# Performance work log

Measured on AMD Instinct MI355X. Metric: run time of the kernel, lower is better.

Reference implementation:

```python
import jax, jax.numpy as jnp
import numpy as np

N_A, N_B = 50000, 20000   # authors, teams
E0, E1, E2 = 600000, 300000, 300000  # coauthor(A->A), writes(A->B), influences(B->A)
D = 128                   # in_feats = out_feats


def setup_inputs() -> dict:
    key = jax.random.key(0)
    ks = jax.random.split(key, 12)
    h_A = jax.random.normal(ks[0], (N_A, D), jnp.float32)
    h_B = jax.random.normal(ks[1], (N_B, D), jnp.float32)
    W0 = jax.random.normal(ks[2], (D, D), jnp.float32) * 0.05
    W1 = jax.random.normal(ks[3], (D, D), jnp.float32) * 0.05
    W2 = jax.random.normal(ks[4], (D, D), jnp.float32) * 0.05
    b0 = jnp.zeros((D,), jnp.float32)
    b1 = jnp.zeros((D,), jnp.float32)
    b2 = jnp.zeros((D,), jnp.float32)
    src0 = jax.random.randint(ks[5], (E0,), 0, N_A)
    dst0 = jax.random.randint(ks[6], (E0,), 0, N_A)
    src1 = jax.random.randint(ks[7], (E1,), 0, N_A)
    dst1 = jax.random.randint(ks[8], (E1,), 0, N_B)
    src2 = jax.random.randint(ks[9], (E2,), 0, N_B)
    dst2 = jax.random.randint(ks[10], (E2,), 0, N_A)
    return dict(h_A=h_A, h_B=h_B, W0=W0, b0=b0, W1=W1, b1=b1, W2=W2, b2=b2,
                src0=src0, dst0=dst0, src1=src1, dst1=dst1, src2=src2, dst2=dst2)


def _graph_conv(x_src, W, b, src, dst, n_dst):
    """DGL GraphConv, norm='both': out = D_dst^{-1/2} A D_src^{-1/2} (X W) + b."""
    n_src = x_src.shape[0]
    ones = jnp.ones(src.shape[0], x_src.dtype)
    deg_out = jnp.clip(jax.ops.segment_sum(ones, src, num_segments=n_src), 1.0)
    deg_in = jnp.clip(jax.ops.segment_sum(ones, dst, num_segments=n_dst), 1.0)
    m = (x_src @ W) * (deg_out ** -0.5)[:, None]          # [n_src, D]
    agg = jax.ops.segment_sum(m[src], dst, num_segments=n_dst)  # [n_dst, D]
    return agg * (deg_in ** -0.5)[:, None] + b


def reference(h_A, h_B, W0, b0, W1, b1, W2, b2, src0, dst0, src1, dst1, src2, dst2):
    # HeteroGraphConv(aggregate='sum'): sum per-relation GraphConv outputs per dst ntype.
    out_A = (_graph_conv(h_A, W0, b0, src0, dst0, N_A)
             + _graph_conv(h_B, W2, b2, src2, dst2, N_A))
    out_B = _graph_conv(h_A, W1, b1, src1, dst1, N_B)
    # every ntype present in h receives an output, so no passthrough branch fires
    return out_A, out_B
```

## Files before the change

kernel.cpp:

```cpp
#include <hip/hip_runtime.h>

#define NA 50000
#define NB 20000
#define NE0 600000
#define NE1 300000
#define NE2 300000
#define DD 128
#define SUB 32768
#define PER 18750


typedef short bf16x8 __attribute__((ext_vector_type(8)));
typedef float f32x4 __attribute__((ext_vector_type(4)));

__device__ __forceinline__ unsigned short f2bf(float f) {
    union { float f; unsigned int u; } v; v.f = f;
    unsigned int r = v.u + 0x7fffu + ((v.u >> 16) & 1u);
    return (unsigned short)(r >> 16);
}
__device__ __forceinline__ float lo2f(unsigned int u) {
    union { float f; unsigned int u; } v; v.u = u << 16;
    return v.f;
}
__device__ __forceinline__ float hi2f(unsigned int u) {
    union { float f; unsigned int u; } v; v.u = u & 0xffff0000u;
    return v.f;
}

__global__ __launch_bounds__(1024) void hist_kernel(
    const int* __restrict__ s0, const int* __restrict__ d0,
    const int* __restrict__ s1, const int* __restrict__ d1,
    const int* __restrict__ s2, const int* __restrict__ d2,
    unsigned int* __restrict__ Pd,
    unsigned char* __restrict__ rank0, unsigned char* __restrict__ rank1,
    unsigned char* __restrict__ rank2,
    const float* __restrict__ W0, const float* __restrict__ W1,
    const float* __restrict__ W2, unsigned short* __restrict__ Wt)
{
    __shared__ unsigned int h32[SUB / 2];
    const int cfg = blockIdx.z;
    if (cfg == 6) {
        int flat = blockIdx.y * 2 + blockIdx.x;
        if (flat >= 48) return;
        int i = flat * 1024 + threadIdx.x;
        int w = i >> 14, r = i & (DD * DD - 1);
        int c = r >> 7, k = r & (DD - 1);
        const float* W = (w == 0) ? W0 : ((w == 1) ? W1 : W2);
        Wt[i] = f2bf(W[k * DD + c]);
        return;
    }
    const int En[6] = {NE0, NE0, NE1, NE1, NE2, NE2};
    const int Kn[6] = {NA, NA, NA, NB, NB, NA};
    const int Gn[6] = {32, 32, 16, 16, 16, 16};
    const int Po[6] = {0, 1600000, 3200000, 4000000, 4320000, 4640000};
    int E = En[cfg], K = Kn[cfg], G = Gn[cfg];
    int sub = blockIdx.x, g = blockIdx.y;
    int nsub = (K + SUB - 1) / SUB;
    if (sub >= nsub || g >= G) return;
    const int* keys = cfg == 0 ? s0 : cfg == 1 ? d0 : cfg == 2 ? s1
                    : cfg == 3 ? d1 : cfg == 4 ? s2 : d2;
    unsigned char* rk = cfg == 1 ? rank0 : cfg == 3 ? rank1
                      : cfg == 5 ? rank2 : (unsigned char*)0;
    int lo = sub * SUB;
    int hi = min(K, lo + SUB);
    int cnt = hi - lo;
    for (int i = threadIdx.x; i < SUB / 2; i += 1024) h32[i] = 0;
    __syncthreads();
    int e1 = min(E, g * PER + PER);
    for (int e = g * PER + threadIdx.x; e < e1; e += 1024) {
        int k = keys[e];
        if (k >= lo && k < hi) {
            int kk = k - lo;
            unsigned sh = (kk & 1) << 4;
            unsigned old = atomicAdd(&h32[kk >> 1], 1u << sh);
            if (rk) rk[e] = (unsigned char)((old >> sh) & 0xffu);
        }
    }
    __syncthreads();
    unsigned int* outp = Pd + ((Po[cfg] + g * K + lo) >> 1);
    for (int i = threadIdx.x; i < cnt / 2; i += 1024) outp[i] = h32[i];
}

__global__ __launch_bounds__(256) void reduce2(
    const unsigned short* __restrict__ P16, int* __restrict__ ideg,
    float* __restrict__ rdeg, int* __restrict__ spart,
    unsigned char* __restrict__ cum8)
{
    __shared__ int lds[256];
    const int y = blockIdx.y;
    const int Ro[6] = {0, NA, 2 * NA, 3 * NA, 3 * NA + NB, 3 * NA + 2 * NB};
    const int Kr[6] = {NA, NA, NA, NB, NB, NA};
    const int Gr[6] = {32, 32, 16, 16, 16, 16};
    const int Po[6] = {0, 1600000, 3200000, 4000000, 4320000, 4640000};
    const int Co[6] = {0, 0, 0, 1600000, 0, 1920000};
    int K = Kr[y], G = Gr[y];
    int b = blockIdx.x, t = threadIdx.x;
    int nchunk = (K + 255) >> 8;
    if (b >= nchunk) return;
    int key = b * 256 + t;
    bool valid = key < K;
    bool din = (y == 1) || (y == 3) || (y == 5);
    const unsigned short* p = P16 + Po[y] + key;
    unsigned char* cb = cum8 + Co[y] + key;
    int run = 0;
    for (int g = 0; g < G; ++g) {
        if (din && valid) cb[g * K] = (unsigned char)run;
        run += valid ? p[g * K] : 0;
    }
    if (valid) {
        ideg[Ro[y] + key] = run;
        rdeg[Ro[y] + key] = rsqrtf(fmaxf((float)run, 1.f));
    }
    if (din) {
        int slot = (y - 1) >> 1;
        lds[t] = run; __syncthreads();
        for (int o = 128; o > 0; o >>= 1) {
            if (t < o) lds[t] += lds[t + o];
            __syncthreads();
        }
        if (t == 0) spart[slot * 256 + b] = lds[0];
    }
}

__global__ __launch_bounds__(256) void scan3(
    const int* __restrict__ ideg, const int* __restrict__ spart,
    int* __restrict__ rp)
{
    __shared__ int lds[256];
    const int y = blockIdx.y;
    const int off[3] = {NA, 3 * NA, 3 * NA + 2 * NB};
    const int nn[3]  = {NA, NB, NA};
    const int ro[3]  = {0, NA, NA + NB};
    int n = nn[y];
    int b = blockIdx.x, t = threadIdx.x;
    if (b * 1024 >= n) return;

    lds[t] = (t < 4 * b) ? spart[y * 256 + t] : 0;
    __syncthreads();
    for (int o = 128; o > 0; o >>= 1) {
        if (t < o) lds[t] += lds[t + o];
        __syncthreads();
    }
    int pv = lds[0];
    __syncthreads();

    const int* deg = ideg + off[y];
    int base = b * 1024 + t * 4;
    int v[4]; int tsum = 0;
    #pragma unroll
    for (int k = 0; k < 4; ++k) {
        v[k] = (base + k < n) ? deg[base + k] : 0;
        tsum += v[k];
    }
    lds[t] = tsum; __syncthreads();
    for (int o = 1; o < 256; o <<= 1) {
        int x = (t >= o) ? lds[t - o] : 0;
        __syncthreads();
        lds[t] += x;
        __syncthreads();
    }
    int run = lds[t] - tsum + pv;
    int* rowptr = rp + ro[y];
    #pragma unroll
    for (int k = 0; k < 4; ++k) {
        if (base + k < n) rowptr[base + k] = run;
        run += v[k];
    }
}

__global__ __launch_bounds__(512) void work_kernel(
    const int* __restrict__ s0, const int* __restrict__ d0,
    const int* __restrict__ s1, const int* __restrict__ d1,
    const int* __restrict__ s2, const int* __restrict__ d2,
    const unsigned char* __restrict__ cum8,
    const unsigned char* __restrict__ rank0, const unsigned char* __restrict__ rank1,
    const unsigned char* __restrict__ rank2,
    const int* __restrict__ rp,
    int* __restrict__ csr0, int* __restrict__ csr1, int* __restrict__ csr2,
    const float* __restrict__ hA, const float* __restrict__ hB,
    const unsigned short* __restrict__ Wt, const float* __restrict__ rdeg,
    unsigned short* __restrict__ mA0, unsigned short* __restrict__ mA1,
    unsigned short* __restrict__ mB2)
{
    int bx = blockIdx.x;
    if (bx < 2344) {
        int z = (bx < 1172) ? 0 : (bx < 1758) ? 1 : 2;
        const int zb[3] = {0, 1172, 1758};
        const int En[3] = {NE0, NE1, NE2};
        const int Kn[3] = {NA, NB, NA};
        const int Co[3] = {0, 1600000, 1920000};
        const int ro[3] = {0, NA, NA + NB};
        int E = En[z], K = Kn[z];
        const int* src = z == 0 ? s0 : z == 1 ? s1 : s2;
        const int* dst = z == 0 ? d0 : z == 1 ? d1 : d2;
        const unsigned char* rk = z == 0 ? rank0 : z == 1 ? rank1 : rank2;
        int* csr = z == 0 ? csr0 : z == 1 ? csr1 : csr2;
        int e = (bx - zb[z]) * 512 + threadIdx.x;
        if (e >= E) return;
        int d = dst[e];
        int g = e / PER;
        int pos = rp[ro[z] + d] + (int)cum8[Co[z] + g * K + d] + (int)rk[e];
        csr[pos] = src[e];
        return;
    }
    int wid  = threadIdx.x >> 6;
    int lane = threadIdx.x & 63;
    int quad = lane >> 4;
    int l16  = lane & 15;
    if (bx < 2344 + 391) {
        int base = (bx - 2344) * 128 + wid * 16;
        if (base >= NA) return;
        int arow = base + l16;
        if (arow >= NA) arow = NA - 1;
        bf16x8 a[4];
        #pragma unroll
        for (int kk = 0; kk < 4; ++kk) {
            const float4* p = (const float4*)(hA + (size_t)arow * DD + kk * 32 + quad * 8);
            float4 u = p[0], w = p[1];
            bf16x8 t;
            t[0] = (short)f2bf(u.x); t[1] = (short)f2bf(u.y);
            t[2] = (short)f2bf(u.z); t[3] = (short)f2bf(u.w);
            t[4] = (short)f2bf(w.x); t[5] = (short)f2bf(w.y);
            t[6] = (short)f2bf(w.z); t[7] = (short)f2bf(w.w);
            a[kk] = t;
        }
        float rs0[4], rs1[4]; int orow0 = base + quad * 4;
        #pragma unroll
        for (int r = 0; r < 4; ++r) {
            int orow = orow0 + r; int c = orow < NA ? orow : 0;
            rs0[r] = rdeg[c]; rs1[r] = rdeg[2 * NA + c];
        }
        #pragma unroll
        for (int ct = 0; ct < 8; ++ct) {
            f32x4 acc0 = {0.f, 0.f, 0.f, 0.f};
            f32x4 acc1 = {0.f, 0.f, 0.f, 0.f};
            const unsigned short* wp = Wt + (size_t)(ct * 16 + l16) * DD + quad * 8;
            #pragma unroll
            for (int kk = 0; kk < 4; ++kk) {
                bf16x8 b0 = *(const bf16x8*)(wp + kk * 32);
                bf16x8 b1 = *(const bf16x8*)(wp + 16384 + kk * 32);
                acc0 = __builtin_amdgcn_mfma_f32_16x16x32_bf16(a[kk], b0, acc0, 0, 0, 0);
                acc1 = __builtin_amdgcn_mfma_f32_16x16x32_bf16(a[kk], b1, acc1, 0, 0, 0);
            }
            #pragma unroll
            for (int r = 0; r < 4; ++r) {
                int orow = orow0 + r;
                if (orow < NA) {
                    mA0[(size_t)orow * DD + ct * 16 + l16] = f2bf(acc0[r] * rs0[r]);
                    mA1[(size_t)orow * DD + ct * 16 + l16] = f2bf(acc1[r] * rs1[r]);
                }
            }
        }
    } else {
        int base = (bx - 2735) * 128 + wid * 16;
        if (base >= NB) return;
        int arow = base + l16;
        if (arow >= NB) arow = NB - 1;
        bf16x8 a[4];
        #pragma unroll
        for (int kk = 0; kk < 4; ++kk) {
            const float4* p = (const float4*)(hB + (size_t)arow * DD + kk * 32 + quad * 8);
            float4 u = p[0], w = p[1];
            bf16x8 t;
            t[0] = (short)f2bf(u.x); t[1] = (short)f2bf(u.y);
            t[2] = (short)f2bf(u.z); t[3] = (short)f2bf(u.w);
            t[4] = (short)f2bf(w.x); t[5] = (short)f2bf(w.y);
            t[6] = (short)f2bf(w.z); t[7] = (short)f2bf(w.w);
            a[kk] = t;
        }
        float rs[4]; int orow0 = base + quad * 4;
        #pragma unroll
        for (int r = 0; r < 4; ++r) {
            int orow = orow0 + r;
            rs[r] = rdeg[3 * NA + NB + (orow < NB ? orow : 0)];
        }
        #pragma unroll
        for (int ct = 0; ct < 8; ++ct) {
            f32x4 acc = {0.f, 0.f, 0.f, 0.f};
            const unsigned short* wp = Wt + 32768 + (size_t)(ct * 16 + l16) * DD + quad * 8;
            #pragma unroll
            for (int kk = 0; kk < 4; ++kk) {
                bf16x8 b = *(const bf16x8*)(wp + kk * 32);
                acc = __builtin_amdgcn_mfma_f32_16x16x32_bf16(a[kk], b, acc, 0, 0, 0);
            }
            #pragma unroll
            for (int r = 0; r < 4; ++r) {
                int orow = orow0 + r;
                if (orow < NB)
                    mB2[(size_t)orow * DD + ct * 16 + l16] = f2bf(acc[r] * rs[r]);
            }
        }
    }
}

__device__ __forceinline__ void acc8(float* o, uint4 u) {
    o[0] += lo2f(u.x); o[1] += hi2f(u.x);
    o[2] += lo2f(u.y); o[3] += hi2f(u.y);
    o[4] += lo2f(u.z); o[5] += hi2f(u.z);
    o[6] += lo2f(u.w); o[7] += hi2f(u.w);
}
__device__ __forceinline__ void gather_rel4(
    const char* __restrict__ Mb, const int* __restrict__ csr,
    int st, int n, int lane, int q, unsigned laneoff, float* o)
{
    for (int ch = 0; ch < n; ch += 64) {
        int m = n - ch; if (m > 64) m = 64;
        int idx = csr[st + ch + (lane < m ? lane : m - 1)];
        int j = 0;
        for (; j + 8 <= m; j += 8) {
            int sA = __shfl(idx, j + q);
            int sB = __shfl(idx, j + 4 + q);
            uint4 uA = *(const uint4*)(Mb + (((unsigned)sA << 8) + laneoff));
            uint4 uB = *(const uint4*)(Mb + (((unsigned)sB << 8) + laneoff));
            acc8(o, uA); acc8(o, uB);
        }
        if (j + 4 <= m) {
            int s = __shfl(idx, j + q);
            uint4 u = *(const uint4*)(Mb + (((unsigned)s << 8) + laneoff));
            acc8(o, u);
            j += 4;
        }
        if (j < m) {
            int jj = j + q;
            float w = jj < m ? 1.f : 0.f;
            int s = __shfl(idx, jj < m ? jj : m - 1);
            uint4 u = *(const uint4*)(Mb + (((unsigned)s << 8) + laneoff));
            o[0] = fmaf(w, lo2f(u.x), o[0]); o[1] = fmaf(w, hi2f(u.x), o[1]);
            o[2] = fmaf(w, lo2f(u.y), o[2]); o[3] = fmaf(w, hi2f(u.y), o[3]);
            o[4] = fmaf(w, lo2f(u.z), o[4]); o[5] = fmaf(w, hi2f(u.z), o[5]);
            o[6] = fmaf(w, lo2f(u.w), o[6]); o[7] = fmaf(w, hi2f(u.w), o[7]);
        }
    }
}

__global__ __launch_bounds__(256) void gather_all(
    const unsigned short* __restrict__ mA0, const unsigned short* __restrict__ mA1,
    const unsigned short* __restrict__ mB2,
    const int* __restrict__ csr0, const int* __restrict__ csr1,
    const int* __restrict__ csr2,
    const int* __restrict__ rp, const int* __restrict__ ideg,
    const float* __restrict__ rdeg,
    const float* __restrict__ b0, const float* __restrict__ b1,
    const float* __restrict__ b2,
    float* __restrict__ out)
{
    int wid = threadIdx.x >> 6, lane = threadIdx.x & 63;
    int q = lane >> 4, l16 = lane & 15;
    unsigned laneoff = (unsigned)l16 * 16u;
    float v[8];
    #pragma unroll
    for (int i = 0; i < 8; ++i) v[i] = 0.f;
    float* op;
    const float *bia, *bib;

    if (blockIdx.x < 12500) {
        int d = blockIdx.x * 4 + wid;
        float c[8];
        #pragma unroll
        for (int i = 0; i < 8; ++i) c[i] = 0.f;
        gather_rel4((const char*)mA0, csr0, rp[d], ideg[NA + d], lane, q, laneoff, v);
        gather_rel4((const char*)mB2, csr2, rp[NA + NB + d], ideg[3 * NA + 2 * NB + d],
                    lane, q, laneoff, c);
        float r0 = rdeg[NA + d], r2 = rdeg[3 * NA + 2 * NB + d];
        #pragma unroll
        for (int i = 0; i < 8; ++i) v[i] = v[i] * r0 + c[i] * r2;
        op = out + (size_t)d * DD;
        bia = b0; bib = b2;
    } else {
        int d = (blockIdx.x - 12500) * 4 + wid;
        gather_rel4((const char*)mA1, csr1, rp[NA + d], ideg[3 * NA + d],
                    lane, q, laneoff, v);
        float r1 = rdeg[3 * NA + d];
        #pragma unroll
        for (int i = 0; i < 8; ++i) v[i] *= r1;
        op = out + (size_t)(NA + d) * DD;
        bia = b1; bib = 0;
    }

    #pragma unroll
    for (int i = 0; i < 8; ++i) {
        v[i] += __shfl_down(v[i], 32);
        v[i] += __shfl_down(v[i], 16);
    }
    if (lane < 16) {
        int col = l16 * 8;
        float4 ba0 = *(const float4*)(bia + col);
        float4 ba1 = *(const float4*)(bia + col + 4);
        if (bib) {
            float4 bb0 = *(const float4*)(bib + col);
            float4 bb1 = *(const float4*)(bib + col + 4);
            ba0.x += bb0.x; ba0.y += bb0.y; ba0.z += bb0.z; ba0.w += bb0.w;
            ba1.x += bb1.x; ba1.y += bb1.y; ba1.z += bb1.z; ba1.w += bb1.w;
        }
        float4 o0 = {v[0] + ba0.x, v[1] + ba0.y, v[2] + ba0.z, v[3] + ba0.w};
        float4 o1 = {v[4] + ba1.x, v[5] + ba1.y, v[6] + ba1.z, v[7] + ba1.w};
        *(float4*)(op + col) = o0;
        *(float4*)(op + col + 4) = o1;
    }
}

extern "C" void kernel_launch(void* const* d_in, const int* in_sizes, int n_in,
                              void* d_out, int out_size, void* d_ws, size_t ws_size,
                              hipStream_t stream) {
    const float* hA = (const float*)d_in[0];
    const float* hB = (const float*)d_in[1];
    const float* W0 = (const float*)d_in[2];
    const float* b0 = (const float*)d_in[3];
    const float* W1 = (const float*)d_in[4];
    const float* b1 = (const float*)d_in[5];
    const float* W2 = (const float*)d_in[6];
    const float* b2 = (const float*)d_in[7];
    const int* s0 = (const int*)d_in[8];
    const int* d0 = (const int*)d_in[9];
    const int* s1 = (const int*)d_in[10];
    const int* d1 = (const int*)d_in[11];
    const int* s2 = (const int*)d_in[12];
    const int* d2 = (const int*)d_in[13];
    float* out = (float*)d_out;
    char* ws = (char*)d_ws;

    unsigned short* mA0 = (unsigned short*)(ws + 0);
    unsigned short* mA1 = (unsigned short*)(ws + 12800000);
    unsigned short* mB2 = (unsigned short*)(ws + 25600000);
    unsigned short* P16 = (unsigned short*)(ws + 0);
    unsigned int*   Pd  = (unsigned int*)(ws + 0);
    unsigned short* Wt  = (unsigned short*)(ws + 30720000);
    float* rdeg         = (float*)(ws + 30818304);
    int*   ideg         = (int*)  (ws + 31778304);
    int*   rp           = (int*)  (ws + 32738304);
    int*   spart        = (int*)  (ws + 33218304);
    unsigned char* cum8 = (unsigned char*)(ws + 33221376);
    unsigned char* rank0= (unsigned char*)(ws + 35941376);
    unsigned char* rank1= (unsigned char*)(ws + 36541376);
    unsigned char* rank2= (unsigned char*)(ws + 36841376);
    int*   csr0         = (int*)  (ws + 37141376);
    int*   csr1         = (int*)  (ws + 39541376);
    int*   csr2         = (int*)  (ws + 40741376);

    hist_kernel<<<dim3(2, 32, 7), 1024, 0, stream>>>(s0, d0, s1, d1, s2, d2,
        Pd, rank0, rank1, rank2, W0, W1, W2, Wt);
    reduce2<<<dim3(196, 6), 256, 0, stream>>>(P16, ideg, rdeg, spart, cum8);
    scan3<<<dim3(49, 3), 256, 0, stream>>>(ideg, spart, rp);
    work_kernel<<<2892, 512, 0, stream>>>(s0, d0, s1, d1, s2, d2,
        cum8, rank0, rank1, rank2, rp, csr0, csr1, csr2,
        hA, hB, Wt, rdeg, mA0, mA1, mB2);
    gather_all<<<12500 + 5000, 256, 0, stream>>>(mA0, mA1, mB2,
        csr0, csr1, csr2, rp, ideg, rdeg, b0, b1, b2, out);
}
```

Measured before the change: 239.6 us.

## Build CSR with LDS atomic cursors and 16-bit column indices, dropping rank arrays

The per-edge rank bytes written by the histogram kernel are removed. CSR fill now runs in blocks that each own a destination sub-range and an edge group, seed LDS cursors from rowptr plus cum8, and claim slots with LDS atomics. CSR source indices are stored as 16-bit values, which halves CSR traffic in both the fill and the gather. The cost is that each fill block rescans its edge group once per sub-range, and edge order within a row is no longer deterministic. Sources for A (up to 50000) still fit in unsigned short.

After: 243.1 us. Within noise of the previous version (+1.5%).

```diff
diff --git a/kernel.cpp b/kernel.cpp
--- a/kernel.cpp
+++ b/kernel.cpp
@@ -8,6 +8,7 @@
 #define DD 128
 #define SUB 32768
 #define PER 18750
+#define PSUB 8192
 
 
 typedef short bf16x8 __attribute__((ext_vector_type(8)));
@@ -32,8 +33,6 @@
     const int* __restrict__ s1, const int* __restrict__ d1,
     const int* __restrict__ s2, const int* __restrict__ d2,
     unsigned int* __restrict__ Pd,
-    unsigned char* __restrict__ rank0, unsigned char* __restrict__ rank1,
-    unsigned char* __restrict__ rank2,
     const float* __restrict__ W0, const float* __restrict__ W1,
     const float* __restrict__ W2, unsigned short* __restrict__ Wt)
 {
@@ -59,8 +58,6 @@
     if (sub >= nsub || g >= G) return;
     const int* keys = cfg == 0 ? s0 : cfg == 1 ? d0 : cfg == 2 ? s1
                     : cfg == 3 ? d1 : cfg == 4 ? s2 : d2;
-    unsigned char* rk = cfg == 1 ? rank0 : cfg == 3 ? rank1
-                      : cfg == 5 ? rank2 : (unsigned char*)0;
     int lo = sub * SUB;
     int hi = min(K, lo + SUB);
     int cnt = hi - lo;
@@ -71,9 +68,7 @@
         int k = keys[e];
         if (k >= lo && k < hi) {
             int kk = k - lo;
-            unsigned sh = (kk & 1) << 4;
-            unsigned old = atomicAdd(&h32[kk >> 1], 1u << sh);
-            if (rk) rk[e] = (unsigned char)((old >> sh) & 0xffu);
+            atomicAdd(&h32[kk >> 1], 1u << ((kk & 1) << 4));
         }
     }
     __syncthreads();
@@ -172,43 +167,22 @@
     const int* __restrict__ s0, const int* __restrict__ d0,
     const int* __restrict__ s1, const int* __restrict__ d1,
     const int* __restrict__ s2, const int* __restrict__ d2,
-    const unsigned char* __restrict__ cum8,
-    const unsigned char* __restrict__ rank0, const unsigned char* __restrict__ rank1,
-    const unsigned char* __restrict__ rank2,
-    const int* __restrict__ rp,
-    int* __restrict__ csr0, int* __restrict__ csr1, int* __restrict__ csr2,
+    const unsigned char* __restrict__ cum8, const int* __restrict__ rp,
+    unsigned short* __restrict__ csr0, unsigned short* __restrict__ csr1,
+    unsigned short* __restrict__ csr2,
     const float* __restrict__ hA, const float* __restrict__ hB,
     const unsigned short* __restrict__ Wt, const float* __restrict__ rdeg,
     unsigned short* __restrict__ mA0, unsigned short* __restrict__ mA1,
     unsigned short* __restrict__ mB2)
 {
+    __shared__ int cnt_lds[PSUB];
     int bx = blockIdx.x;
-    if (bx < 2344) {
-        int z = (bx < 1172) ? 0 : (bx < 1758) ? 1 : 2;
-        const int zb[3] = {0, 1172, 1758};
-        const int En[3] = {NE0, NE1, NE2};
-        const int Kn[3] = {NA, NB, NA};
-        const int Co[3] = {0, 1600000, 1920000};
-        const int ro[3] = {0, NA, NA + NB};
-        int E = En[z], K = Kn[z];
-        const int* src = z == 0 ? s0 : z == 1 ? s1 : s2;
-        const int* dst = z == 0 ? d0 : z == 1 ? d1 : d2;
-        const unsigned char* rk = z == 0 ? rank0 : z == 1 ? rank1 : rank2;
-        int* csr = z == 0 ? csr0 : z == 1 ? csr1 : csr2;
-        int e = (bx - zb[z]) * 512 + threadIdx.x;
-        if (e >= E) return;
-        int d = dst[e];
-        int g = e / PER;
-        int pos = rp[ro[z] + d] + (int)cum8[Co[z] + g * K + d] + (int)rk[e];
-        csr[pos] = src[e];
-        return;
-    }
     int wid  = threadIdx.x >> 6;
     int lane = threadIdx.x & 63;
     int quad = lane >> 4;
     int l16  = lane & 15;
-    if (bx < 2344 + 391) {
-        int base = (bx - 2344) * 128 + wid * 16;
+    if (bx < 391) {
+        int base = bx * 128 + wid * 16;
         if (base >= NA) return;
         int arow = base + l16;
         if (arow >= NA) arow = NA - 1;
@@ -251,8 +225,10 @@
                 }
             }
         }
-    } else {
-        int base = (bx - 2735) * 128 + wid * 16;
+        return;
+    }
+    if (bx < 548) {
+        int base = (bx - 391) * 128 + wid * 16;
         if (base >= NB) return;
         int arow = base + l16;
         if (arow >= NB) arow = NB - 1;
@@ -290,6 +266,36 @@
                     mB2[(size_t)orow * DD + ct * 16 + l16] = f2bf(acc[r] * rs[r]);
             }
         }
+        return;
+    }
+    int pb = bx - 548;
+    int z, g, sub;
+    if (pb < 224)      { z = 0; g = pb / 7;          sub = pb % 7; }
+    else if (pb < 272) { z = 1; g = (pb - 224) / 3;  sub = (pb - 224) % 3; }
+    else               { z = 2; g = (pb - 272) / 7;  sub = (pb - 272) % 7; }
+    const int En[3] = {NE0, NE1, NE2};
+    const int Kn[3] = {NA, NB, NA};
+    const int Co[3] = {0, 1600000, 1920000};
+    const int ro[3] = {0, NA, NA + NB};
+    int E = En[z], K = Kn[z];
+    const int* src = z == 0 ? s0 : z == 1 ? s1 : s2;
+    const int* dst = z == 0 ? d0 : z == 1 ? d1 : d2;
+    unsigned short* csr = z == 0 ? csr0 : z == 1 ? csr1 : csr2;
+    int lo = sub * PSUB;
+    int hi = min(K, lo + PSUB);
+    int cnt = hi - lo;
+    const int* rpz = rp + ro[z] + lo;
+    const unsigned char* cz = cum8 + Co[z] + (size_t)g * K + lo;
+    for (int i = threadIdx.x; i < cnt; i += 512)
+        cnt_lds[i] = rpz[i] + (int)cz[i];
+    __syncthreads();
+    int e1 = min(E, g * PER + PER);
+    for (int e = g * PER + threadIdx.x; e < e1; e += 512) {
+        int d = dst[e];
+        if (d >= lo && d < hi) {
+            int pos = atomicAdd(&cnt_lds[d - lo], 1);
+            csr[pos] = (unsigned short)src[e];
+        }
     }
 }
 
@@ -300,7 +306,7 @@
     o[6] += lo2f(u.w); o[7] += hi2f(u.w);
 }
 __device__ __forceinline__ void gather_rel4(
-    const char* __restrict__ Mb, const int* __restrict__ csr,
+    const char* __restrict__ Mb, const unsigned short* __restrict__ csr,
     int st, int n, int lane, int q, unsigned laneoff, float* o)
 {
     for (int ch = 0; ch < n; ch += 64) {
@@ -336,8 +342,8 @@
 __global__ __launch_bounds__(256) void gather_all(
     const unsigned short* __restrict__ mA0, const unsigned short* __restrict__ mA1,
     const unsigned short* __restrict__ mB2,
-    const int* __restrict__ csr0, const int* __restrict__ csr1,
-    const int* __restrict__ csr2,
+    const unsigned short* __restrict__ csr0, const unsigned short* __restrict__ csr1,
+    const unsigned short* __restrict__ csr2,
     const int* __restrict__ rp, const int* __restrict__ ideg,
     const float* __restrict__ rdeg,
     const float* __restrict__ b0, const float* __restrict__ b1,
@@ -430,19 +436,16 @@
     int*   rp           = (int*)  (ws + 32738304);
     int*   spart        = (int*)  (ws + 33218304);
     unsigned char* cum8 = (unsigned char*)(ws + 33221376);
-    unsigned char* rank0= (unsigned char*)(ws + 35941376);
-    unsigned char* rank1= (unsigned char*)(ws + 36541376);
-    unsigned char* rank2= (unsigned char*)(ws + 36841376);
-    int*   csr0         = (int*)  (ws + 37141376);
-    int*   csr1         = (int*)  (ws + 39541376);
-    int*   csr2         = (int*)  (ws + 40741376);
+    unsigned short* csr0= (unsigned short*)(ws + 35941376);
+    unsigned short* csr1= (unsigned short*)(ws + 37141376);
+    unsigned short* csr2= (unsigned short*)(ws + 37741376);
 
     hist_kernel<<<dim3(2, 32, 7), 1024, 0, stream>>>(s0, d0, s1, d1, s2, d2,
-        Pd, rank0, rank1, rank2, W0, W1, W2, Wt);
+        Pd, W0, W1, W2, Wt);
     reduce2<<<dim3(196, 6), 256, 0, stream>>>(P16, ideg, rdeg, spart, cum8);
     scan3<<<dim3(49, 3), 256, 0, stream>>>(ideg, spart, rp);
-    work_kernel<<<2892, 512, 0, stream>>>(s0, d0, s1, d1, s2, d2,
-        cum8, rank0, rank1, rank2, rp, csr0, csr1, csr2,
+    work_kernel<<<548 + 384, 512, 0, stream>>>(s0, d0, s1, d1, s2, d2,
+        cum8, rp, csr0, csr1, csr2,
         hA, hB, Wt, rdeg, mA0, mA1, mB2);
     gather_all<<<12500 + 5000, 256, 0, stream>>>(mA0, mA1, mB2,
         csr0, csr1, csr2, rp, ideg, rdeg, b0, b1, b2, out);
```
